# Optimization experiments

Hardware: AMD Instinct MI355X
Metric: run time of the kernel (lower is better)

## Reference

```python
import jax, jax.numpy as jnp
import numpy as np

B, T, C, V = 8, 2048, 256, 1024


def setup_inputs() -> dict:
    key = jax.random.key(0)
    k1, k2 = jax.random.split(key)
    z = jax.random.normal(k1, (B, T, C), dtype=jnp.float32)
    codebook = jax.random.normal(k2, (V, C), dtype=jnp.float32)
    mask = jnp.ones((B, T, 1), dtype=jnp.float32)
    return {"z": z, "codebook": codebook, "mask": mask}


def reference(z, codebook, mask):
    # e = codebook.embedding.weight.clone().detach()
    e = jax.lax.stop_gradient(codebook)            # (V, C)
    b, t, c = z.shape
    v = e.shape[0]
    zf = z.reshape(-1, c)                          # (B*T, C)
    # squared distances: ||z||^2 + ||e||^2 - 2 z e^T
    d = (jnp.sum(zf * zf, axis=1, keepdims=True)
         + jnp.sum(e * e, axis=1)
         - 2.0 * zf @ e.T)                         # (B*T, V)
    idx = jnp.argmin(d, axis=1)                    # (B*T,)
    # one-hot scatter + matmul gather == direct gather
    z_q = e[idx].reshape(b, t, c)
    z_q = z_q * mask
    pad_e = e[0]                                   # (C,)
    z_q = jnp.where(mask == 0, pad_e, z_q)
    # masked MSE commitment loss
    valid_count = jnp.sum(mask) * c
    commitment_loss = jnp.sum((z - jax.lax.stop_gradient(z_q)) ** 2 * mask) / valid_count
    # straight-through estimator
    z_q = z + jax.lax.stop_gradient(z_q - z)
    min_encoding_indices = idx.reshape(b, t)
    # run-length dedup (deterministic: keep first element of each run),
    # compacted to the front and padded with pad_e to static length T
    keep = jnp.concatenate(
        [jnp.ones((b, 1), bool),
         min_encoding_indices[:, 1:] != min_encoding_indices[:, :-1]], axis=1)
    order = jnp.argsort(jnp.where(keep, 0, 1), axis=1, stable=True)  # kept positions first
    gathered = jnp.take_along_axis(z_q, order[:, :, None], axis=1)
    kept_sorted = jnp.take_along_axis(keep, order, axis=1)
    z_q_disc = jnp.where(kept_sorted[:, :, None], gathered, pad_e)
    # softmax diversity loss over soft assignments
    soft = jax.nn.softmax(-d, axis=1)              # (B*T, V)
    hist = jnp.sum(soft * mask.reshape(-1, 1), axis=0)  # (V,)
    p = hist / (jnp.sum(hist) + 1e-8)
    diversity_loss = jnp.sum(p * jnp.log(p * v + 1e-8))
    return (commitment_loss, diversity_loss, z_q, z_q_disc, min_encoding_indices)
```

## Files before the change

kernel.cpp:

```cpp
#include <hip/hip_runtime.h>
#include <math.h>

#define NB 8
#define NT 2048
#define NC 256
#define NV 1024
#define BT (NB*NT)

typedef __attribute__((ext_vector_type(8)))  short bf16x8;
typedef __attribute__((ext_vector_type(8)))  short short8v;
typedef __attribute__((ext_vector_type(16))) float f32x16;

#define HIST_OFF  0
#define EN_OFF    4096
#define CPART_OFF 8192
#define MPART_OFF 12288
#define ORD_OFF   16384
#define KC_OFF    49152
#define WS_REQ    49184

__device__ __forceinline__ float bf_hi(float v, short* bits) {
  unsigned u = __float_as_uint(v);
  *bits = (short)(u >> 16);
  return __uint_as_float(u & 0xffff0000u);
}

__global__ __launch_bounds__(256) void vq_prep_e(
    const float* __restrict__ e, short* __restrict__ e1,
    short* __restrict__ e2, short* __restrict__ e3, float* __restrict__ en)
{
  __shared__ float el[32 * NC];
  const int t = threadIdx.x, cb = blockIdx.x;
  {
    const int r = t >> 3, cc = (t & 7) * 32;
    const float* er = e + (size_t)(cb * 32 + r) * NC + cc;
    float* dst = el + r * NC + cc;
    float ss = 0.f;
    #pragma unroll
    for (int i = 0; i < 8; ++i) {
      float4 v = *(const float4*)(er + i * 4);
      *(float4*)(dst + i * 4) = v;
      ss += v.x * v.x + v.y * v.y + v.z * v.z + v.w * v.w;
    }
    #pragma unroll
    for (int off = 1; off < 8; off <<= 1) ss += __shfl_xor(ss, off, 64);
    if ((t & 7) == 0) en[cb * 32 + r] = ss;
  }
  __syncthreads();
  const int s = t >> 4, h = (t >> 3) & 1, rb = (t & 7) * 4;
  const int kb = s * 16 + h * 8;
  #pragma unroll
  for (int rr = 0; rr < 4; ++rr) {
    short8v p1, p2, p3;
    #pragma unroll
    for (int ii = 0; ii < 8; ++ii) {
      float v = el[(rb + rr) * NC + kb + ii];
      short b1, b2, b3;
      float f1 = bf_hi(v, &b1);
      float r1 = v - f1;
      float f2 = bf_hi(r1, &b2);
      float r2 = r1 - f2;
      bf_hi(r2, &b3);
      p1[ii] = b1; p2[ii] = b2; p3[ii] = b3;
    }
    size_t off = (size_t)(s * 2 + h) * 8192 + (size_t)(cb * 32 + rb + rr) * 8;
    *(short8v*)(e1 + off) = p1;
    *(short8v*)(e2 + off) = p2;
    *(short8v*)(e3 + off) = p3;
  }
}

__global__ __launch_bounds__(1024, 1) void vq_main_fused(
    const float* __restrict__ z,
    const short* __restrict__ eT1, const short* __restrict__ eT2, const short* __restrict__ eT3,
    const float* __restrict__ en, const float* __restrict__ mask,
    float* __restrict__ hist, float* __restrict__ idxf)
{
  __shared__ short zl1[16384], zl2[16384], zl3[16384];
  __shared__ float pmv[64][8];
  __shared__ int   pmi[64][8];
  __shared__ float psum[64][8];
  __shared__ float mfin[64];
  __shared__ float wrow[64];

  const int tid  = threadIdx.x;
  const int lane = tid & 63, wv = tid >> 6;
  const int l31  = lane & 31, half = lane >> 5;
  const int mt   = wv >> 3, nq = wv & 7;
  const int b = blockIdx.x, row0 = b * 64;

  {
    const int s = wv, r = lane;
    const float* zp = z + (size_t)(row0 + r) * NC + s * 16;
    float v[16];
    #pragma unroll
    for (int i = 0; i < 4; ++i) *(float4*)(v + i * 4) = *(const float4*)(zp + i * 4);
    #pragma unroll
    for (int hh = 0; hh < 2; ++hh) {
      short8v p1, p2, p3;
      #pragma unroll
      for (int ii = 0; ii < 8; ++ii) {
        float x = v[hh * 8 + ii];
        short b1, b2, b3;
        float f1 = bf_hi(x, &b1);
        float r1 = x - f1;
        float f2 = bf_hi(r1, &b2);
        float r2 = r1 - f2;
        bf_hi(r2, &b3);
        p1[ii] = b1; p2[ii] = b2; p3[ii] = b3;
      }
      const int off = (s * 2 + hh) * 512 + r * 8;
      *(short8v*)&zl1[off] = p1;
      *(short8v*)&zl2[off] = p2;
      *(short8v*)&zl3[off] = p3;
    }
  }
  __syncthreads();

  f32x16 acc[4];
  #pragma unroll
  for (int t = 0; t < 4; ++t)
    #pragma unroll
    for (int r = 0; r < 16; ++r) acc[t][r] = 0.f;

  const int sb = b & 15;
  #pragma unroll
  for (int ss = 0; ss < 16; ++ss) {
    const int s = (ss + sb) & 15;
    const int aoff = (s * 2 + half) * 512 + (mt * 32 + l31) * 8;
    const bf16x8 a1 = *(const bf16x8*)&zl1[aoff];
    const bf16x8 a2 = *(const bf16x8*)&zl2[aoff];
    const bf16x8 a3 = *(const bf16x8*)&zl3[aoff];
    const size_t bbase = (size_t)(s * 2 + half) * 8192 + (size_t)(nq * 128 + l31) * 8;
    #pragma unroll
    for (int t = 0; t < 4; ++t) {
      const size_t bo = bbase + (size_t)(t * 32) * 8;
      const bf16x8 b1 = *(const bf16x8*)(eT1 + bo);
      const bf16x8 b2 = *(const bf16x8*)(eT2 + bo);
      const bf16x8 b3 = *(const bf16x8*)(eT3 + bo);
      acc[t] = __builtin_amdgcn_mfma_f32_32x32x16_bf16(a1, b1, acc[t], 0, 0, 0);
      acc[t] = __builtin_amdgcn_mfma_f32_32x32x16_bf16(a2, b1, acc[t], 0, 0, 0);
      acc[t] = __builtin_amdgcn_mfma_f32_32x32x16_bf16(a3, b1, acc[t], 0, 0, 0);
      acc[t] = __builtin_amdgcn_mfma_f32_32x32x16_bf16(a1, b2, acc[t], 0, 0, 0);
      acc[t] = __builtin_amdgcn_mfma_f32_32x32x16_bf16(a2, b2, acc[t], 0, 0, 0);
      acc[t] = __builtin_amdgcn_mfma_f32_32x32x16_bf16(a1, b3, acc[t], 0, 0, 0);
    }
  }

  float enr[4];
  #pragma unroll
  for (int t = 0; t < 4; ++t) enr[t] = en[nq * 128 + t * 32 + l31];
  #pragma unroll
  for (int t = 0; t < 4; ++t)
    #pragma unroll
    for (int r = 0; r < 16; ++r) acc[t][r] = fmaf(-2.f, acc[t][r], enr[t]);

  float bv[16]; int bi[16];
  #pragma unroll
  for (int r = 0; r < 16; ++r) {
    bv[r] = acc[0][r]; bi[r] = nq * 128 + l31;
    #pragma unroll
    for (int t = 1; t < 4; ++t) {
      float vv = acc[t][r]; int cc = nq * 128 + t * 32 + l31;
      if (vv < bv[r]) { bv[r] = vv; bi[r] = cc; }
    }
    #pragma unroll
    for (int off = 1; off <= 16; off <<= 1) {
      float ov = __shfl_xor(bv[r], off, 64);
      int   oi = __shfl_xor(bi[r], off, 64);
      if (ov < bv[r] || (ov == bv[r] && oi < bi[r])) { bv[r] = ov; bi[r] = oi; }
    }
  }
  if (l31 == 0) {
    #pragma unroll
    for (int r = 0; r < 16; ++r) {
      int rowb = mt * 32 + (r & 3) + 8 * (r >> 2) + 4 * half;
      pmv[rowb][nq] = bv[r]; pmi[rowb][nq] = bi[r];
    }
  }
  __syncthreads();
  if (tid < 64) {
    float mv = pmv[tid][0]; int mi = pmi[tid][0];
    #pragma unroll
    for (int w = 1; w < 8; ++w) {
      float v = pmv[tid][w]; int i2 = pmi[tid][w];
      if (v < mv || (v == mv && i2 < mi)) { mv = v; mi = i2; }
    }
    mfin[tid] = mv;
    idxf[row0 + tid] = (float)mi;
  }
  __syncthreads();

  #pragma unroll
  for (int r = 0; r < 16; ++r) {
    const int rowb = mt * 32 + (r & 3) + 8 * (r >> 2) + 4 * half;
    float m = mfin[rowb];
    float s0 = 0.f;
    #pragma unroll
    for (int t = 0; t < 4; ++t) {
      float p = __expf(m - acc[t][r]);
      acc[t][r] = p; s0 += p;
    }
    #pragma unroll
    for (int off = 1; off <= 16; off <<= 1) s0 += __shfl_xor(s0, off, 64);
    if (l31 == 0) psum[rowb][nq] = s0;
  }
  __syncthreads();
  if (tid < 64) {
    float s0 = 0.f;
    #pragma unroll
    for (int w = 0; w < 8; ++w) s0 += psum[tid][w];
    wrow[tid] = mask[row0 + tid] / s0;
  }
  __syncthreads();

  #pragma unroll
  for (int t = 0; t < 4; ++t) {
    float h = 0.f;
    #pragma unroll
    for (int r = 0; r < 16; ++r)
      h = fmaf(wrow[mt * 32 + (r & 3) + 8 * (r >> 2) + 4 * half], acc[t][r], h);
    h += __shfl_xor(h, 32, 64);
    if (half == 0 && h > 1e-12f) atomicAdd(&hist[nq * 128 + t * 32 + l31], h);
  }
}

__global__ __launch_bounds__(256) void vq_gather(
    const float* __restrict__ z, const float* __restrict__ e,
    const float* __restrict__ mask, const float* __restrict__ idxf,
    float* __restrict__ zq, float* __restrict__ cpart, float* __restrict__ mpart)
{
  const int tid = threadIdx.x, bid = blockIdx.x;
  float cacc = 0.f, macc = 0.f;
  #pragma unroll
  for (int it = 0; it < 4; ++it) {
    int id  = bid * 1024 + it * 256 + tid;
    int row = id >> 6;
    int c4  = (id & 63) << 2;
    int idx = (int)idxf[row];
    float mv = mask[row];
    float4 zv = *(const float4*)(z + (size_t)row * NC + c4);
    float4 qv;
    if (mv == 0.0f) {
      qv = *(const float4*)(e + c4);
    } else {
      float4 ev = *(const float4*)(e + (size_t)idx * NC + c4);
      qv = make_float4(ev.x * mv, ev.y * mv, ev.z * mv, ev.w * mv);
    }
    *(float4*)(zq + (size_t)row * NC + c4) = qv;
    float dx = zv.x - qv.x, dy = zv.y - qv.y, dz = zv.z - qv.z, dw = zv.w - qv.w;
    cacc += (dx * dx + dy * dy + dz * dz + dw * dw) * mv;
    macc += mv;
  }
  #pragma unroll
  for (int off = 32; off; off >>= 1) {
    cacc += __shfl_down(cacc, off, 64);
    macc += __shfl_down(macc, off, 64);
  }
  __shared__ float w4[4], m4[4];
  if ((tid & 63) == 0) { w4[tid >> 6] = cacc; m4[tid >> 6] = macc; }
  __syncthreads();
  if (tid == 0) {
    cpart[bid] = w4[0] + w4[1] + w4[2] + w4[3];
    mpart[bid] = (m4[0] + m4[1] + m4[2] + m4[3]) * (1.0f / 64.0f);
  }
}

__global__ void vq_scan(const float* __restrict__ idxf, unsigned short* __restrict__ ord,
                        int* __restrict__ Kc) {
  int b = blockIdx.x, t = threadIdx.x;
  const float* ix = idxf + b * NT;
  int flags[8]; int cnt = 0; int base = t * 8;
  #pragma unroll
  for (int i = 0; i < 8; ++i) {
    int g = base + i;
    int k = (g == 0) ? 1 : (ix[g] != ix[g - 1] ? 1 : 0);
    flags[i] = k; cnt += k;
  }
  int lane = t & 63, wv = t >> 6;
  int scan = cnt;
  for (int off = 1; off < 64; off <<= 1) {
    int v = __shfl_up(scan, off, 64);
    if (lane >= off) scan += v;
  }
  __shared__ int wsum[4];
  if (lane == 63) wsum[wv] = scan;
  __syncthreads();
  int woff = 0;
  for (int w = 0; w < wv; ++w) woff += wsum[w];
  int pos = woff + scan - cnt;
  #pragma unroll
  for (int i = 0; i < 8; ++i) {
    if (flags[i]) { ord[b * NT + pos] = (unsigned short)(base + i); ++pos; }
  }
  if (t == 255) Kc[b] = woff + scan;
}

__global__ __launch_bounds__(256) void vq_disc(
    const float* __restrict__ zq, const float* __restrict__ e,
    const unsigned short* __restrict__ ord, const int* __restrict__ Kc,
    float* __restrict__ disc)
{
  const int tid = threadIdx.x, bid = blockIdx.x;
  #pragma unroll
  for (int it = 0; it < 2; ++it) {
    int id  = bid * 512 + it * 256 + tid;
    int row = id >> 6;
    int c4  = (id & 63) << 2;
    int b   = row >> 11;
    int j   = row & (NT - 1);
    int K   = Kc[b];
    float4 v;
    if (j < K) {
      int src = ord[(b << 11) + j];
      v = *(const float4*)(zq + ((size_t)(b << 11) + src) * NC + c4);
    } else {
      v = *(const float4*)(e + c4);
    }
    *(float4*)(disc + (size_t)row * NC + c4) = v;
  }
}

__global__ void vq_final(const float* __restrict__ hist, const float* __restrict__ cpart,
                         const float* __restrict__ mpart, float* __restrict__ out) {
  int t = threadIdx.x;
  double csum = 0, msum = 0, hsum = 0;
  #pragma unroll
  for (int i = 0; i < 4; ++i) {
    csum += (double)cpart[i * 256 + t];
    msum += (double)mpart[i * 256 + t];
  }
  double h[4];
  #pragma unroll
  for (int i = 0; i < 4; ++i) { h[i] = (double)hist[i * 256 + t]; hsum += h[i]; }
  #pragma unroll
  for (int off = 32; off; off >>= 1) {
    csum += __shfl_down(csum, off, 64);
    msum += __shfl_down(msum, off, 64);
    hsum += __shfl_down(hsum, off, 64);
  }
  __shared__ double wc[4], wm[4], wh[4];
  __shared__ double tots[3];
  if ((t & 63) == 0) { int w = t >> 6; wc[w] = csum; wm[w] = msum; wh[w] = hsum; }
  __syncthreads();
  if (t == 0) {
    tots[0] = wc[0] + wc[1] + wc[2] + wc[3];
    tots[1] = wm[0] + wm[1] + wm[2] + wm[3];
    tots[2] = wh[0] + wh[1] + wh[2] + wh[3];
  }
  __syncthreads();
  double tot = tots[2] + 1e-8;
  double dv = 0;
  #pragma unroll
  for (int i = 0; i < 4; ++i) {
    double p = h[i] / tot;
    dv += p * log(p * 1024.0 + 1e-8);
  }
  #pragma unroll
  for (int off = 32; off; off >>= 1) dv += __shfl_down(dv, off, 64);
  if ((t & 63) == 0) wc[t >> 6] = dv;
  __syncthreads();
  if (t == 0) {
    out[1] = (float)(wc[0] + wc[1] + wc[2] + wc[3]);
    out[0] = (float)(tots[0] / (tots[1] * 256.0));
  }
}

extern "C" void kernel_launch(void* const* d_in, const int* in_sizes, int n_in,
                              void* d_out, int out_size, void* d_ws, size_t ws_size,
                              hipStream_t stream) {
  if (ws_size < (size_t)WS_REQ) return;

  const float* z    = (const float*)d_in[0];
  const float* e    = (const float*)d_in[1];
  const float* mask = (const float*)d_in[2];
  float* out = (float*)d_out;
  char* ws = (char*)d_ws;

  float*          hist  = (float*)(ws + HIST_OFF);
  float*          en    = (float*)(ws + EN_OFF);
  float*          cpart = (float*)(ws + CPART_OFF);
  float*          mpart = (float*)(ws + MPART_OFF);
  unsigned short* ord   = (unsigned short*)(ws + ORD_OFF);
  int*            Kc    = (int*)(ws + KC_OFF);

  float* zq   = out + 2;
  float* disc = out + 2 + (size_t)BT * NC;
  float* idxf = out + 2 + (size_t)2 * BT * NC;

  short* e1 = (short*)disc;
  short* e2 = e1 + (size_t)NV * NC;
  short* e3 = e2 + (size_t)NV * NC;

  hipMemsetAsync(ws + HIST_OFF, 0, 4096, stream);
  vq_prep_e    <<<32, 256, 0, stream>>>(e, e1, e2, e3, en);
  vq_main_fused<<<256, 1024, 0, stream>>>(z, e1, e2, e3, en, mask, hist, idxf);
  vq_gather    <<<1024, 256, 0, stream>>>(z, e, mask, idxf, zq, cpart, mpart);
  vq_scan      <<<NB, 256, 0, stream>>>(idxf, ord, Kc);
  vq_disc      <<<2048, 256, 0, stream>>>(zq, e, ord, Kc, disc);
  vq_final     <<<1, NC, 0, stream>>>(hist, cpart, mpart, out);
}
```

Baseline: 167.9 us.

## Split main VQ kernel into 32-row blocks and double-buffer operand loads

The fused distance/argmin/softmax kernel now processes 32 rows per 512-thread block instead of 64 rows per 1024-thread block, launching 512 blocks with two allowed per CU. The MFMA k-loop is restructured with register double buffering, so the next slice's A (LDS) and B (global) fragments load while the current slice's MFMAs run. The B operands are read from global memory by each block, so halving the rows per block doubles total codebook traffic. It also drops the per-block slice rotation, and the doubled operand registers may pressure occupancy.

```diff
diff --git a/kernel.cpp b/kernel.cpp
--- a/kernel.cpp
+++ b/kernel.cpp
@@ -70,27 +70,53 @@
   }
 }
 
-__global__ __launch_bounds__(1024, 1) void vq_main_fused(
+#define LOAD_A(dst, s_) {                                               \
+    const int aoff_ = (s_) * 512 + half * 256 + l31 * 8;                \
+    dst[0] = *(const bf16x8*)&zl1[aoff_];                               \
+    dst[1] = *(const bf16x8*)&zl2[aoff_];                               \
+    dst[2] = *(const bf16x8*)&zl3[aoff_]; }
+
+#define LOAD_B(dst, s_) {                                               \
+    const size_t bb_ = (size_t)((s_) * 2 + half) * 8192                 \
+                     + (size_t)(nq * 128 + l31) * 8;                    \
+    _Pragma("unroll")                                                   \
+    for (int t_ = 0; t_ < 4; ++t_) {                                    \
+      const size_t bo_ = bb_ + (size_t)(t_ * 32) * 8;                   \
+      dst[t_][0] = *(const bf16x8*)(eT1 + bo_);                         \
+      dst[t_][1] = *(const bf16x8*)(eT2 + bo_);                         \
+      dst[t_][2] = *(const bf16x8*)(eT3 + bo_); } }
+
+#define MFMA_STEP(za, eb) {                                                        \
+    _Pragma("unroll")                                                              \
+    for (int t_ = 0; t_ < 4; ++t_) {                                               \
+      acc[t_] = __builtin_amdgcn_mfma_f32_32x32x16_bf16(za[0], eb[t_][0], acc[t_], 0, 0, 0); \
+      acc[t_] = __builtin_amdgcn_mfma_f32_32x32x16_bf16(za[1], eb[t_][0], acc[t_], 0, 0, 0); \
+      acc[t_] = __builtin_amdgcn_mfma_f32_32x32x16_bf16(za[2], eb[t_][0], acc[t_], 0, 0, 0); \
+      acc[t_] = __builtin_amdgcn_mfma_f32_32x32x16_bf16(za[0], eb[t_][1], acc[t_], 0, 0, 0); \
+      acc[t_] = __builtin_amdgcn_mfma_f32_32x32x16_bf16(za[1], eb[t_][1], acc[t_], 0, 0, 0); \
+      acc[t_] = __builtin_amdgcn_mfma_f32_32x32x16_bf16(za[0], eb[t_][2], acc[t_], 0, 0, 0); } }
+
+__global__ __launch_bounds__(512, 2) void vq_main_fused(
     const float* __restrict__ z,
     const short* __restrict__ eT1, const short* __restrict__ eT2, const short* __restrict__ eT3,
     const float* __restrict__ en, const float* __restrict__ mask,
     float* __restrict__ hist, float* __restrict__ idxf)
 {
-  __shared__ short zl1[16384], zl2[16384], zl3[16384];
-  __shared__ float pmv[64][8];
-  __shared__ int   pmi[64][8];
-  __shared__ float psum[64][8];
-  __shared__ float mfin[64];
-  __shared__ float wrow[64];
+  __shared__ short zl1[8192], zl2[8192], zl3[8192];
+  __shared__ float pmv[32][8];
+  __shared__ int   pmi[32][8];
+  __shared__ float psum[32][8];
+  __shared__ float mfin[32];
+  __shared__ float wrow[32];
 
   const int tid  = threadIdx.x;
   const int lane = tid & 63, wv = tid >> 6;
   const int l31  = lane & 31, half = lane >> 5;
-  const int mt   = wv >> 3, nq = wv & 7;
-  const int b = blockIdx.x, row0 = b * 64;
+  const int nq   = wv;
+  const int b = blockIdx.x, row0 = b * 32;
 
   {
-    const int s = wv, r = lane;
+    const int s = tid >> 5, r = tid & 31;
     const float* zp = z + (size_t)(row0 + r) * NC + s * 16;
     float v[16];
     #pragma unroll
@@ -109,7 +135,7 @@
         bf_hi(r2, &b3);
         p1[ii] = b1; p2[ii] = b2; p3[ii] = b3;
       }
-      const int off = (s * 2 + hh) * 512 + r * 8;
+      const int off = s * 512 + hh * 256 + r * 8;
       *(short8v*)&zl1[off] = p1;
       *(short8v*)&zl2[off] = p2;
       *(short8v*)&zl3[off] = p3;
@@ -123,28 +149,15 @@
     #pragma unroll
     for (int r = 0; r < 16; ++r) acc[t][r] = 0.f;
 
-  const int sb = b & 15;
-  #pragma unroll
-  for (int ss = 0; ss < 16; ++ss) {
-    const int s = (ss + sb) & 15;
-    const int aoff = (s * 2 + half) * 512 + (mt * 32 + l31) * 8;
-    const bf16x8 a1 = *(const bf16x8*)&zl1[aoff];
-    const bf16x8 a2 = *(const bf16x8*)&zl2[aoff];
-    const bf16x8 a3 = *(const bf16x8*)&zl3[aoff];
-    const size_t bbase = (size_t)(s * 2 + half) * 8192 + (size_t)(nq * 128 + l31) * 8;
-    #pragma unroll
-    for (int t = 0; t < 4; ++t) {
-      const size_t bo = bbase + (size_t)(t * 32) * 8;
-      const bf16x8 b1 = *(const bf16x8*)(eT1 + bo);
-      const bf16x8 b2 = *(const bf16x8*)(eT2 + bo);
-      const bf16x8 b3 = *(const bf16x8*)(eT3 + bo);
-      acc[t] = __builtin_amdgcn_mfma_f32_32x32x16_bf16(a1, b1, acc[t], 0, 0, 0);
-      acc[t] = __builtin_amdgcn_mfma_f32_32x32x16_bf16(a2, b1, acc[t], 0, 0, 0);
-      acc[t] = __builtin_amdgcn_mfma_f32_32x32x16_bf16(a3, b1, acc[t], 0, 0, 0);
-      acc[t] = __builtin_amdgcn_mfma_f32_32x32x16_bf16(a1, b2, acc[t], 0, 0, 0);
-      acc[t] = __builtin_amdgcn_mfma_f32_32x32x16_bf16(a2, b2, acc[t], 0, 0, 0);
-      acc[t] = __builtin_amdgcn_mfma_f32_32x32x16_bf16(a1, b3, acc[t], 0, 0, 0);
-    }
+  bf16x8 zA[3], zB[3];
+  bf16x8 eA[4][3], eB[4][3];
+  LOAD_A(zA, 0); LOAD_B(eA, 0);
+  #pragma unroll
+  for (int s = 0; s < 16; s += 2) {
+    LOAD_A(zB, s + 1); LOAD_B(eB, s + 1);
+    MFMA_STEP(zA, eA);
+    if (s < 14) { LOAD_A(zA, s + 2); LOAD_B(eA, s + 2); }
+    MFMA_STEP(zB, eB);
   }
 
   float enr[4];
@@ -174,12 +187,12 @@
   if (l31 == 0) {
     #pragma unroll
     for (int r = 0; r < 16; ++r) {
-      int rowb = mt * 32 + (r & 3) + 8 * (r >> 2) + 4 * half;
+      int rowb = (r & 3) + 8 * (r >> 2) + 4 * half;
       pmv[rowb][nq] = bv[r]; pmi[rowb][nq] = bi[r];
     }
   }
   __syncthreads();
-  if (tid < 64) {
+  if (tid < 32) {
     float mv = pmv[tid][0]; int mi = pmi[tid][0];
     #pragma unroll
     for (int w = 1; w < 8; ++w) {
@@ -193,7 +206,7 @@
 
   #pragma unroll
   for (int r = 0; r < 16; ++r) {
-    const int rowb = mt * 32 + (r & 3) + 8 * (r >> 2) + 4 * half;
+    const int rowb = (r & 3) + 8 * (r >> 2) + 4 * half;
     float m = mfin[rowb];
     float s0 = 0.f;
     #pragma unroll
@@ -206,7 +219,7 @@
     if (l31 == 0) psum[rowb][nq] = s0;
   }
   __syncthreads();
-  if (tid < 64) {
+  if (tid < 32) {
     float s0 = 0.f;
     #pragma unroll
     for (int w = 0; w < 8; ++w) s0 += psum[tid][w];
@@ -219,7 +232,7 @@
     float h = 0.f;
     #pragma unroll
     for (int r = 0; r < 16; ++r)
-      h = fmaf(wrow[mt * 32 + (r & 3) + 8 * (r >> 2) + 4 * half], acc[t][r], h);
+      h = fmaf(wrow[(r & 3) + 8 * (r >> 2) + 4 * half], acc[t][r], h);
     h += __shfl_xor(h, 32, 64);
     if (half == 0 && h > 1e-12f) atomicAdd(&hist[nq * 128 + t * 32 + l31], h);
   }
@@ -394,7 +407,7 @@
 
   hipMemsetAsync(ws + HIST_OFF, 0, 4096, stream);
   vq_prep_e    <<<32, 256, 0, stream>>>(e, e1, e2, e3, en);
-  vq_main_fused<<<256, 1024, 0, stream>>>(z, e1, e2, e3, en, mask, hist, idxf);
+  vq_main_fused<<<512, 512, 0, stream>>>(z, e1, e2, e3, en, mask, hist, idxf);
   vq_gather    <<<1024, 256, 0, stream>>>(z, e, mask, idxf, zq, cpart, mpart);
   vq_scan      <<<NB, 256, 0, stream>>>(idxf, ord, Kc);
   vq_disc      <<<2048, 256, 0, stream>>>(zq, e, ord, Kc, disc);
```

New measurement: 184.6 us. 1.1x slower.
